# Optimization experiments

Measured on AMD Instinct MI355X. Metric: run time of the kernel, lower is better.

Reference implementation:

```python
import jax, jax.numpy as jnp
import numpy as np

N, M, D, H = 256, 1024, 512, 512


def setup_inputs() -> dict:
    key = jax.random.key(0)
    k1, k2, k3, k4 = jax.random.split(key, 4)
    scale = 1.0 / np.sqrt(D)
    return {
        "embeddings": jax.random.normal(k1, (N, D), dtype=jnp.float32),
        "support_tensors": jax.random.normal(k2, (M, D), dtype=jnp.float32),
        "W1": jax.random.normal(k3, (D, H), dtype=jnp.float32) * scale,
        "b1": jnp.zeros((H,), dtype=jnp.float32),
        "W2": jax.random.normal(k4, (H, 1), dtype=jnp.float32) * (1.0 / np.sqrt(H)),
        "b2": jnp.zeros((1,), dtype=jnp.float32),
    }


def reference(embeddings, support_tensors, W1, b1, W2, b2):
    # SupportLayer.call: tile queries x support set into all N*M pairs,
    # apply pairwise kernel (siamese head: sigmoid(MLP(|a - b|))),
    # reshape back to similarity matrix [N, M].
    # Broadcasting replaces the explicit tf.tile / reshape.
    diff = jnp.abs(embeddings[:, None, :] - support_tensors[None, :, :])  # [N, M, D]
    h = jax.nn.relu(jnp.einsum("nmd,dh->nmh", diff, W1) + b1)             # [N, M, H]
    logits = jnp.einsum("nmh,ho->nmo", h, W2)[..., 0] + b2[0]             # [N, M]
    return jax.nn.sigmoid(logits)
```

## Files before the change

### kernel.cpp

```cpp
#include <hip/hip_runtime.h>
#include <hip/hip_bf16.h>

#define N_Q 256
#define M_S 1024
#define DD 512
#define HH 512

typedef __attribute__((ext_vector_type(8))) short short8;
typedef __attribute__((ext_vector_type(8))) __bf16 bf16x8;
typedef __attribute__((ext_vector_type(16))) float f32x16;
typedef __attribute__((ext_vector_type(2))) __bf16 bf16x2;

union U8 { short8 s; bf16x8 b; };

__device__ __forceinline__ unsigned short f2bf(float f) {
  unsigned int u = __float_as_uint(f);
  u += 0x7FFFu + ((u >> 16) & 1u);
  return (unsigned short)(u >> 16);
}

__device__ __forceinline__ short8 pack8(const float* d) {
#if defined(__has_builtin) && __has_builtin(__builtin_amdgcn_cvt_pk_bf16_f32)
  short8 r;
#pragma unroll
  for (int i = 0; i < 4; ++i) {
    union { bf16x2 v; short s[2]; } u;
    u.v = __builtin_amdgcn_cvt_pk_bf16_f32(d[2 * i], d[2 * i + 1]);
    r[2 * i] = u.s[0];
    r[2 * i + 1] = u.s[1];
  }
  return r;
#else
  short8 r;
#pragma unroll
  for (int i = 0; i < 8; ++i) r[i] = (short)f2bf(d[i]);
  return r;
#endif
}

__device__ __forceinline__ short8 packdiff(float4 e0, float4 e1, float4 s0, float4 s1) {
  float d[8];
  d[0] = fabsf(e0.x - s0.x); d[1] = fabsf(e0.y - s0.y);
  d[2] = fabsf(e0.z - s0.z); d[3] = fabsf(e0.w - s0.w);
  d[4] = fabsf(e1.x - s1.x); d[5] = fabsf(e1.y - s1.y);
  d[6] = fabsf(e1.z - s1.z); d[7] = fabsf(e1.w - s1.w);
  return pack8(d);
}

__global__ __launch_bounds__(512) void prep_w1s(const float* __restrict__ W1,
                                                unsigned short* __restrict__ w1s) {
  const int f = blockIdx.x;
  const int kc = f >> 4, h32 = f & 15;
  const int l = threadIdx.x & 63, j = threadIdx.x >> 6;
  const int h = h32 * 32 + (l & 31);
  const int k = kc * 16 + (l >> 5) * 8 + j;
  w1s[f * 512 + l * 8 + j] = f2bf(W1[k * HH + h]);
}

__global__ __launch_bounds__(512, 4) void support_kernel(
    const float* __restrict__ emb, const float* __restrict__ sup,
    const unsigned short* __restrict__ w1s, const float* __restrict__ b1,
    const float* __restrict__ W2, const float* __restrict__ b2,
    float* __restrict__ out) {
  __shared__ short8 As16[64 * 64];

  const int tid = threadIdx.x;
  const int lane = tid & 63;
  const int wid = tid >> 6;
  const int l31 = lane & 31;
  const int khalf = lane >> 5;

  const int m0 = blockIdx.x * 16;
  const int n0 = blockIdx.y * 4;

  const int c = tid & 63;
  const int rg = tid >> 6;
  const int nl = rg >> 1;
  const int mq = rg & 1;

  const unsigned short* bb = w1s + (wid * 2) * 512 + lane * 8;
  U8 b[3][2];
#pragma unroll
  for (int tj = 0; tj < 2; ++tj) {
    b[0][tj].s = *(const short8*)(bb + (0 * 16 + tj) * 512);
    b[1][tj].s = *(const short8*)(bb + (1 * 16 + tj) * 512);
  }

  {
    const float* ep = emb + (n0 + nl) * DD + c * 8;
    const float4 e0 = *(const float4*)ep;
    const float4 e1 = *(const float4*)(ep + 4);
    const float* sbase = sup + (m0 + mq * 8) * DD + c * 8;
#pragma unroll
    for (int j = 0; j < 8; ++j) {
      const float4 s0 = *(const float4*)(sbase + j * DD);
      const float4 s1 = *(const float4*)(sbase + j * DD + 4);
      const int p = rg * 8 + j;
      As16[p * 64 + (c ^ j)] = packdiff(e0, e1, s0, s1);
    }
  }
  __syncthreads();

  const int ar0 = (0 + l31) * 64;
  const int ar1 = (32 + l31) * 64;
  const int ax = l31 & 7;

  f32x16 acc[2][2] = {};
  U8 a[2][2];
  a[0][0].s = As16[ar0 + (khalf ^ ax)];
  a[0][1].s = As16[ar1 + (khalf ^ ax)];

#pragma unroll
  for (int ks = 0; ks < 32; ++ks) {
    const int cur = ks & 1;
    if (ks < 31) {
      const int cc = ((ks + 1) * 2 + khalf) ^ ax;
      a[cur ^ 1][0].s = As16[ar0 + cc];
      a[cur ^ 1][1].s = As16[ar1 + cc];
    }
    if (ks + 2 < 32) {
#pragma unroll
      for (int tj = 0; tj < 2; ++tj)
        b[(ks + 2) % 3][tj].s = *(const short8*)(bb + ((ks + 2) * 16 + tj) * 512);
    }
#pragma unroll
    for (int am = 0; am < 2; ++am)
#pragma unroll
      for (int tj = 0; tj < 2; ++tj)
        acc[am][tj] = __builtin_amdgcn_mfma_f32_32x32x16_bf16(
            a[cur][am].b, b[ks % 3][tj].b, acc[am][tj], 0, 0, 0);
  }

  float b1v[2], w2v[2];
#pragma unroll
  for (int tj = 0; tj < 2; ++tj) {
    const int h = (wid * 2 + tj) * 32 + l31;
    b1v[tj] = b1[h];
    w2v[tj] = W2[h];
  }
  __syncthreads();
  float* psums = (float*)As16;
#pragma unroll
  for (int am = 0; am < 2; ++am) {
#pragma unroll
    for (int r = 0; r < 16; ++r) {
      float s = fmaxf(acc[am][0][r] + b1v[0], 0.f) * w2v[0] +
                fmaxf(acc[am][1][r] + b1v[1], 0.f) * w2v[1];
      s += __shfl_xor(s, 1, 64);
      s += __shfl_xor(s, 2, 64);
      s += __shfl_xor(s, 4, 64);
      s += __shfl_xor(s, 8, 64);
      s += __shfl_xor(s, 16, 64);
      if (l31 == 0) {
        const int row32 = (r & 3) + 8 * (r >> 2) + 4 * khalf;
        psums[(am * 32 + row32) * 8 + wid] = s;
      }
    }
  }
  __syncthreads();
  if (tid < 64) {
    float t = b2[0];
#pragma unroll
    for (int w = 0; w < 8; ++w) t += psums[tid * 8 + w];
    out[(n0 + (tid >> 4)) * M_S + m0 + (tid & 15)] = 1.f / (1.f + __expf(-t));
  }
}

extern "C" void kernel_launch(void* const* d_in, const int* in_sizes, int n_in,
                              void* d_out, int out_size, void* d_ws, size_t ws_size,
                              hipStream_t stream) {
  const float* emb = (const float*)d_in[0];
  const float* sup = (const float*)d_in[1];
  const float* W1  = (const float*)d_in[2];
  const float* b1  = (const float*)d_in[3];
  const float* W2  = (const float*)d_in[4];
  const float* b2  = (const float*)d_in[5];
  float* out = (float*)d_out;
  unsigned short* w1s = (unsigned short*)d_ws;

  prep_w1s<<<512, 512, 0, stream>>>(W1, w1s);
  support_kernel<<<dim3(M_S / 16, N_Q / 4), 512, 0, stream>>>(
      emb, sup, w1s, b1, W2, b2, out);
}
```

Measured before the change: 228.8 us.

## Double block pair tile, transpose MFMA operands for a cheaper epilogue, raise MFMA priority

Each block now runs 1024 threads covering 8 queries by 16 supports. Two wave groups share each W1 slice, so the B fragments are fetched by more waves per block, and the diff tile moves to 128KB of dynamic LDS. The MFMA operands are swapped so hidden units sit in the register dimension. The ReLU·W2 reduction then happens mostly inside each lane with one cross-half shuffle, replacing 32 rounds of five-step butterfly shuffles. s_setprio is added around the MFMA group. The cost is one block per CU because of the large LDS use, and heavier register and LDS pressure per block.

```diff
diff --git a/kernel.cpp b/kernel.cpp
--- a/kernel.cpp
+++ b/kernel.cpp
@@ -57,28 +57,30 @@
   w1s[f * 512 + l * 8 + j] = f2bf(W1[k * HH + h]);
 }
 
-__global__ __launch_bounds__(512, 4) void support_kernel(
+__global__ __launch_bounds__(1024, 4) void support_kernel(
     const float* __restrict__ emb, const float* __restrict__ sup,
     const unsigned short* __restrict__ w1s, const float* __restrict__ b1,
     const float* __restrict__ W2, const float* __restrict__ b2,
     float* __restrict__ out) {
-  __shared__ short8 As16[64 * 64];
+  extern __shared__ short8 As16[];
 
   const int tid = threadIdx.x;
   const int lane = tid & 63;
   const int wid = tid >> 6;
   const int l31 = lane & 31;
   const int khalf = lane >> 5;
+  const int hslice = wid & 7;
+  const int pgset = wid >> 3;
 
   const int m0 = blockIdx.x * 16;
-  const int n0 = blockIdx.y * 4;
+  const int n0 = blockIdx.y * 8;
 
   const int c = tid & 63;
   const int rg = tid >> 6;
   const int nl = rg >> 1;
   const int mq = rg & 1;
 
-  const unsigned short* bb = w1s + (wid * 2) * 512 + lane * 8;
+  const unsigned short* bb = w1s + (hslice * 2) * 512 + lane * 8;
   U8 b[3][2];
 #pragma unroll
   for (int tj = 0; tj < 2; ++tj) {
@@ -101,8 +103,8 @@
   }
   __syncthreads();
 
-  const int ar0 = (0 + l31) * 64;
-  const int ar1 = (32 + l31) * 64;
+  const int ar0 = (pgset * 64 + 0 + l31) * 64;
+  const int ar1 = (pgset * 64 + 32 + l31) * 64;
   const int ax = l31 & 7;
 
   f32x16 acc[2][2] = {};
@@ -123,45 +125,45 @@
       for (int tj = 0; tj < 2; ++tj)
         b[(ks + 2) % 3][tj].s = *(const short8*)(bb + ((ks + 2) * 16 + tj) * 512);
     }
+    __builtin_amdgcn_s_setprio(1);
 #pragma unroll
     for (int am = 0; am < 2; ++am)
 #pragma unroll
       for (int tj = 0; tj < 2; ++tj)
         acc[am][tj] = __builtin_amdgcn_mfma_f32_32x32x16_bf16(
-            a[cur][am].b, b[ks % 3][tj].b, acc[am][tj], 0, 0, 0);
+            b[ks % 3][tj].b, a[cur][am].b, acc[am][tj], 0, 0, 0);
+    __builtin_amdgcn_s_setprio(0);
   }
 
-  float b1v[2], w2v[2];
+  float s[2];
 #pragma unroll
-  for (int tj = 0; tj < 2; ++tj) {
-    const int h = (wid * 2 + tj) * 32 + l31;
-    b1v[tj] = b1[h];
-    w2v[tj] = W2[h];
+  for (int am = 0; am < 2; ++am) {
+    float sm = 0.f;
+#pragma unroll
+    for (int tj = 0; tj < 2; ++tj) {
+      const float* b1p = b1 + (hslice * 2 + tj) * 32 + khalf * 4;
+      const float* w2p = W2 + (hslice * 2 + tj) * 32 + khalf * 4;
+#pragma unroll
+      for (int rq = 0; rq < 4; ++rq) {
+        const float4 b1q = *(const float4*)(b1p + rq * 8);
+        const float4 w2q = *(const float4*)(w2p + rq * 8);
+        sm += fmaxf(acc[am][tj][rq * 4 + 0] + b1q.x, 0.f) * w2q.x;
+        sm += fmaxf(acc[am][tj][rq * 4 + 1] + b1q.y, 0.f) * w2q.y;
+        sm += fmaxf(acc[am][tj][rq * 4 + 2] + b1q.z, 0.f) * w2q.z;
+        sm += fmaxf(acc[am][tj][rq * 4 + 3] + b1q.w, 0.f) * w2q.w;
+      }
+    }
+    sm += __shfl_xor(sm, 32, 64);
+    s[am] = sm;
   }
   __syncthreads();
   float* psums = (float*)As16;
-#pragma unroll
-  for (int am = 0; am < 2; ++am) {
-#pragma unroll
-    for (int r = 0; r < 16; ++r) {
-      float s = fmaxf(acc[am][0][r] + b1v[0], 0.f) * w2v[0] +
-                fmaxf(acc[am][1][r] + b1v[1], 0.f) * w2v[1];
-      s += __shfl_xor(s, 1, 64);
-      s += __shfl_xor(s, 2, 64);
-      s += __shfl_xor(s, 4, 64);
-      s += __shfl_xor(s, 8, 64);
-      s += __shfl_xor(s, 16, 64);
-      if (l31 == 0) {
-        const int row32 = (r & 3) + 8 * (r >> 2) + 4 * khalf;
-        psums[(am * 32 + row32) * 8 + wid] = s;
-      }
-    }
-  }
+  psums[(pgset * 64 + lane) * 9 + hslice] = khalf ? s[1] : s[0];
   __syncthreads();
-  if (tid < 64) {
+  if (tid < 128) {
     float t = b2[0];
 #pragma unroll
-    for (int w = 0; w < 8; ++w) t += psums[tid * 8 + w];
+    for (int w = 0; w < 8; ++w) t += psums[tid * 9 + w];
     out[(n0 + (tid >> 4)) * M_S + m0 + (tid & 15)] = 1.f / (1.f + __expf(-t));
   }
 }
@@ -178,7 +180,14 @@
   float* out = (float*)d_out;
   unsigned short* w1s = (unsigned short*)d_ws;
 
+  static bool attr_done = false;
+  if (!attr_done) {
+    hipFuncSetAttribute((const void*)support_kernel,
+                        hipFuncAttributeMaxDynamicSharedMemorySize, 131072);
+    attr_done = true;
+  }
+
   prep_w1s<<<512, 512, 0, stream>>>(W1, w1s);
-  support_kernel<<<dim3(M_S / 16, N_Q / 4), 512, 0, stream>>>(
+  support_kernel<<<dim3(M_S / 16, N_Q / 8), 1024, 131072, stream>>>(
       emb, sup, w1s, b1, W2, b2, out);
 }
```

New measurement: 212.7 us. 7.0% less time.
